# Optimization experiments

Measured on AMD Instinct MI355X. Metric: run time of the kernel, lower is better.

## Reference

```python
import jax, jax.numpy as jnp
import numpy as np

M = 131072  # KV length
DK = 256    # key dim
DV = 256    # value dim


def setup_inputs() -> dict:
    key = jax.random.key(0)
    k1, k2, k3 = jax.random.split(key, 3)
    q = jax.random.normal(k1, (DK,), dtype=jnp.float32)
    K = jax.random.normal(k2, (M, DK), dtype=jnp.float32)
    V = jax.random.normal(k3, (M, DV), dtype=jnp.float32)
    return {"q": q, "K": K, "V": V}


def reference(q, K, V):
    # logits[m] = sum_k K[m,k] * q[k]
    logits = jnp.einsum('mk,k->m', K, q)
    # stable softmax over the m axis
    weights = jax.nn.softmax(logits, axis=-1)
    # y[v] = sum_m weights[m] * V[m,v]
    return jnp.einsum('m,mv->v', weights, V)
```

## Files before the change

kernel.cpp:

```cpp
#include <hip/hip_runtime.h>
#include <math.h>

#define DKD 256
#define DVD 256

constexpr int NB_MAX = 1024;
constexpr int TPB    = 256;
constexpr int WAVES  = TPB / 64;
constexpr int RG     = 64;

__global__ __launch_bounds__(TPB) void attn_pass1(
    const float* __restrict__ q,
    const float* __restrict__ K,
    const float* __restrict__ V,
    float* __restrict__ m_arr,
    float* __restrict__ l_arr,
    float* __restrict__ acc_arr,
    int M, int rows_per_block)
{
    const int lane = threadIdx.x & 63;
    const int wave = threadIdx.x >> 6;
    const int b    = blockIdx.x;

    const float4* __restrict__ K4 = (const float4*)K;
    const float4* __restrict__ V4 = (const float4*)V;
    const float4  q4 = ((const float4*)q)[lane];

    const int row_begin = b * rows_per_block;
    const int row_end   = min(M, row_begin + rows_per_block);

    const int per_wave = (rows_per_block + WAVES - 1) / WAVES;
    const int wbeg = row_begin + wave * per_wave;
    const int wend = min(row_end, wbeg + per_wave);

    float  mx  = -INFINITY;
    float  l   = 0.0f;
    float4 acc = make_float4(0.f, 0.f, 0.f, 0.f);

    for (int r = wbeg; r < wend; r += 4) {
        const int r0 = r;
        const int r1 = min(r + 1, wend - 1);
        const int r2 = min(r + 2, wend - 1);
        const int r3 = min(r + 3, wend - 1);
        const bool v1 = (r + 1 < wend), v2 = (r + 2 < wend), v3 = (r + 3 < wend);

        float4 k0 = K4[(size_t)r0 * 64 + lane];
        float4 k1 = K4[(size_t)r1 * 64 + lane];
        float4 k2 = K4[(size_t)r2 * 64 + lane];
        float4 k3 = K4[(size_t)r3 * 64 + lane];
        float4 w0v = V4[(size_t)r0 * 64 + lane];
        float4 w1v = V4[(size_t)r1 * 64 + lane];
        float4 w2v = V4[(size_t)r2 * 64 + lane];
        float4 w3v = V4[(size_t)r3 * 64 + lane];

        float s0 = k0.x*q4.x + k0.y*q4.y + k0.z*q4.z + k0.w*q4.w;
        float s1 = k1.x*q4.x + k1.y*q4.y + k1.z*q4.z + k1.w*q4.w;
        float s2 = k2.x*q4.x + k2.y*q4.y + k2.z*q4.z + k2.w*q4.w;
        float s3 = k3.x*q4.x + k3.y*q4.y + k3.z*q4.z + k3.w*q4.w;

        #pragma unroll
        for (int off = 32; off > 0; off >>= 1) {
            s0 += __shfl_xor(s0, off);
            s1 += __shfl_xor(s1, off);
            s2 += __shfl_xor(s2, off);
            s3 += __shfl_xor(s3, off);
        }

        if (!v1) s1 = -INFINITY;
        if (!v2) s2 = -INFINITY;
        if (!v3) s3 = -INFINITY;

        const float nm = fmaxf(mx, fmaxf(fmaxf(s0, s1), fmaxf(s2, s3)));
        const float corr = __expf(mx - nm);
        const float e0 = __expf(s0 - nm);
        const float e1 = __expf(s1 - nm);
        const float e2 = __expf(s2 - nm);
        const float e3 = __expf(s3 - nm);

        l = l * corr + (e0 + e1 + e2 + e3);
        acc.x = acc.x * corr + e0*w0v.x + e1*w1v.x + e2*w2v.x + e3*w3v.x;
        acc.y = acc.y * corr + e0*w0v.y + e1*w1v.y + e2*w2v.y + e3*w3v.y;
        acc.z = acc.z * corr + e0*w0v.z + e1*w1v.z + e2*w2v.z + e3*w3v.z;
        acc.w = acc.w * corr + e0*w0v.w + e1*w1v.w + e2*w2v.w + e3*w3v.w;
        mx = nm;
    }

    __shared__ float4 s_acc[WAVES][64];
    __shared__ float  s_mx[WAVES];
    __shared__ float  s_l[WAVES];

    s_acc[wave][lane] = acc;
    if (lane == 0) { s_mx[wave] = mx; s_l[wave] = l; }
    __syncthreads();

    const int t = threadIdx.x;
    float bm = -INFINITY;
    #pragma unroll
    for (int w = 0; w < WAVES; ++w) bm = fmaxf(bm, s_mx[w]);
    if (bm == -INFINITY) bm = 0.0f;

    float yv = 0.0f, bl = 0.0f;
    const float* s_acc_f = (const float*)&s_acc[0][0];
    #pragma unroll
    for (int w = 0; w < WAVES; ++w) {
        const float sc = __expf(s_mx[w] - bm);
        yv += sc * s_acc_f[w * DVD + t];
        bl += sc * s_l[w];
    }

    acc_arr[(size_t)b * DVD + t] = yv;
    if (t == 0) { m_arr[b] = bm; l_arr[b] = bl; }
}

__global__ __launch_bounds__(256) void attn_pass2(
    const float* __restrict__ m_arr,
    const float* __restrict__ l_arr,
    const float* __restrict__ acc_arr,
    float* __restrict__ out,
    int nb, int chunk)
{
    __shared__ float red[256];
    __shared__ float sscale[64];
    const int t = threadIdx.x;

    float lm = -INFINITY;
    for (int b = t; b < nb; b += 256) lm = fmaxf(lm, m_arr[b]);
    red[t] = lm; __syncthreads();
    for (int s = 128; s > 0; s >>= 1) {
        if (t < s) red[t] = fmaxf(red[t], red[t + s]);
        __syncthreads();
    }
    const float Mg = red[0];
    __syncthreads();

    float ll = 0.0f;
    for (int b = t; b < nb; b += 256) ll += l_arr[b] * __expf(m_arr[b] - Mg);
    red[t] = ll; __syncthreads();
    for (int s = 128; s > 0; s >>= 1) {
        if (t < s) red[t] += red[t + s];
        __syncthreads();
    }
    const float invL = 1.0f / red[0];
    __syncthreads();

    const int b0 = blockIdx.x * chunk;
    const int b1 = min(nb, b0 + chunk);
    if (t < b1 - b0) sscale[t] = __expf(m_arr[b0 + t] - Mg);
    __syncthreads();

    float part = 0.0f;
    for (int b = b0; b < b1; ++b)
        part += sscale[b - b0] * acc_arr[(size_t)b * DVD + t];

    atomicAdd(&out[t], part * invL);
}

extern "C" void kernel_launch(void* const* d_in, const int* in_sizes, int n_in,
                              void* d_out, int out_size, void* d_ws, size_t ws_size,
                              hipStream_t stream) {
    const float* q = (const float*)d_in[0];
    const float* K = (const float*)d_in[1];
    const float* V = (const float*)d_in[2];
    float* out = (float*)d_out;

    const int M = in_sizes[1] / DKD;

    int nb = NB_MAX;
    while (nb > 1 && (size_t)nb * (2 + DVD) * sizeof(float) > ws_size) nb >>= 1;
    float* ws     = (float*)d_ws;
    float* m_arr  = ws;
    float* l_arr  = ws + nb;
    float* acc_arr= ws + 2 * nb;

    const int rpb = (M + nb - 1) / nb;

    hipMemsetAsync(d_out, 0, DVD * sizeof(float), stream);
    attn_pass1<<<nb, TPB, 0, stream>>>(q, K, V, m_arr, l_arr, acc_arr, M, rpb);
    const int chunk = (nb + RG - 1) / RG;
    attn_pass2<<<RG, 256, 0, stream>>>(m_arr, l_arr, acc_arr, out, nb, chunk);
}
```

Before: 287.1 us.

## Double block count, split remainder loop, and restructure final reduction per column

```diff
diff --git a/kernel.cpp b/kernel.cpp
--- a/kernel.cpp
+++ b/kernel.cpp
@@ -4,12 +4,11 @@
 #define DKD 256
 #define DVD 256
 
-constexpr int NB_MAX = 1024;
+constexpr int NB_MAX = 2048;
 constexpr int TPB    = 256;
 constexpr int WAVES  = TPB / 64;
-constexpr int RG     = 64;
 
-__global__ __launch_bounds__(TPB) void attn_pass1(
+__global__ __launch_bounds__(TPB, 8) void attn_pass1(
     const float* __restrict__ q,
     const float* __restrict__ K,
     const float* __restrict__ V,
@@ -37,21 +36,19 @@
     float  l   = 0.0f;
     float4 acc = make_float4(0.f, 0.f, 0.f, 0.f);
 
-    for (int r = wbeg; r < wend; r += 4) {
-        const int r0 = r;
-        const int r1 = min(r + 1, wend - 1);
-        const int r2 = min(r + 2, wend - 1);
-        const int r3 = min(r + 3, wend - 1);
-        const bool v1 = (r + 1 < wend), v2 = (r + 2 < wend), v3 = (r + 3 < wend);
+    const int n_rows = wend - wbeg;
+    const int full_end = wbeg + (n_rows & ~3);
 
-        float4 k0 = K4[(size_t)r0 * 64 + lane];
-        float4 k1 = K4[(size_t)r1 * 64 + lane];
-        float4 k2 = K4[(size_t)r2 * 64 + lane];
-        float4 k3 = K4[(size_t)r3 * 64 + lane];
-        float4 w0v = V4[(size_t)r0 * 64 + lane];
-        float4 w1v = V4[(size_t)r1 * 64 + lane];
-        float4 w2v = V4[(size_t)r2 * 64 + lane];
-        float4 w3v = V4[(size_t)r3 * 64 + lane];
+    for (int r = wbeg; r < full_end; r += 4) {
+        const size_t base = (size_t)r * 64 + lane;
+        float4 k0 = K4[base];
+        float4 k1 = K4[base + 64];
+        float4 k2 = K4[base + 128];
+        float4 k3 = K4[base + 192];
+        float4 v0 = V4[base];
+        float4 v1 = V4[base + 64];
+        float4 v2 = V4[base + 128];
+        float4 v3 = V4[base + 192];
 
         float s0 = k0.x*q4.x + k0.y*q4.y + k0.z*q4.z + k0.w*q4.w;
         float s1 = k1.x*q4.x + k1.y*q4.y + k1.z*q4.z + k1.w*q4.w;
@@ -66,10 +63,6 @@
             s3 += __shfl_xor(s3, off);
         }
 
-        if (!v1) s1 = -INFINITY;
-        if (!v2) s2 = -INFINITY;
-        if (!v3) s3 = -INFINITY;
-
         const float nm = fmaxf(mx, fmaxf(fmaxf(s0, s1), fmaxf(s2, s3)));
         const float corr = __expf(mx - nm);
         const float e0 = __expf(s0 - nm);
@@ -78,10 +71,27 @@
         const float e3 = __expf(s3 - nm);
 
         l = l * corr + (e0 + e1 + e2 + e3);
-        acc.x = acc.x * corr + e0*w0v.x + e1*w1v.x + e2*w2v.x + e3*w3v.x;
-        acc.y = acc.y * corr + e0*w0v.y + e1*w1v.y + e2*w2v.y + e3*w3v.y;
-        acc.z = acc.z * corr + e0*w0v.z + e1*w1v.z + e2*w2v.z + e3*w3v.z;
-        acc.w = acc.w * corr + e0*w0v.w + e1*w1v.w + e2*w2v.w + e3*w3v.w;
+        acc.x = acc.x * corr + e0*v0.x + e1*v1.x + e2*v2.x + e3*v3.x;
+        acc.y = acc.y * corr + e0*v0.y + e1*v1.y + e2*v2.y + e3*v3.y;
+        acc.z = acc.z * corr + e0*v0.z + e1*v1.z + e2*v2.z + e3*v3.z;
+        acc.w = acc.w * corr + e0*v0.w + e1*v1.w + e2*v2.w + e3*v3.w;
+        mx = nm;
+    }
+
+    for (int r = full_end; r < wend; ++r) {
+        float4 k0 = K4[(size_t)r * 64 + lane];
+        float4 v0 = V4[(size_t)r * 64 + lane];
+        float s0 = k0.x*q4.x + k0.y*q4.y + k0.z*q4.z + k0.w*q4.w;
+        #pragma unroll
+        for (int off = 32; off > 0; off >>= 1) s0 += __shfl_xor(s0, off);
+        const float nm = fmaxf(mx, s0);
+        const float corr = __expf(mx - nm);
+        const float e0 = __expf(s0 - nm);
+        l = l * corr + e0;
+        acc.x = acc.x * corr + e0*v0.x;
+        acc.y = acc.y * corr + e0*v0.y;
+        acc.z = acc.z * corr + e0*v0.z;
+        acc.w = acc.w * corr + e0*v0.w;
         mx = nm;
     }
 
@@ -117,10 +127,10 @@
     const float* __restrict__ l_arr,
     const float* __restrict__ acc_arr,
     float* __restrict__ out,
-    int nb, int chunk)
+    int nb)
 {
     __shared__ float red[256];
-    __shared__ float sscale[64];
+    __shared__ float sscale[NB_MAX];
     const int t = threadIdx.x;
 
     float lm = -INFINITY;
@@ -134,7 +144,11 @@
     __syncthreads();
 
     float ll = 0.0f;
-    for (int b = t; b < nb; b += 256) ll += l_arr[b] * __expf(m_arr[b] - Mg);
+    for (int b = t; b < nb; b += 256) {
+        const float sc = __expf(m_arr[b] - Mg);
+        sscale[b] = sc;
+        ll += sc * l_arr[b];
+    }
     red[t] = ll; __syncthreads();
     for (int s = 128; s > 0; s >>= 1) {
         if (t < s) red[t] += red[t + s];
@@ -143,16 +157,17 @@
     const float invL = 1.0f / red[0];
     __syncthreads();
 
-    const int b0 = blockIdx.x * chunk;
-    const int b1 = min(nb, b0 + chunk);
-    if (t < b1 - b0) sscale[t] = __expf(m_arr[b0 + t] - Mg);
-    __syncthreads();
+    const int j = blockIdx.x;
+    float part = 0.0f;
+    for (int b = t; b < nb; b += 256)
+        part += sscale[b] * acc_arr[(size_t)b * DVD + j];
 
-    float part = 0.0f;
-    for (int b = b0; b < b1; ++b)
-        part += sscale[b - b0] * acc_arr[(size_t)b * DVD + t];
-
-    atomicAdd(&out[t], part * invL);
+    red[t] = part; __syncthreads();
+    for (int s = 128; s > 0; s >>= 1) {
+        if (t < s) red[t] += red[t + s];
+        __syncthreads();
+    }
+    if (t == 0) out[j] = red[0] * invL;
 }
 
 extern "C" void kernel_launch(void* const* d_in, const int* in_sizes, int n_in,
@@ -167,15 +182,13 @@
 
     int nb = NB_MAX;
     while (nb > 1 && (size_t)nb * (2 + DVD) * sizeof(float) > ws_size) nb >>= 1;
-    float* ws     = (float*)d_ws;
-    float* m_arr  = ws;
-    float* l_arr  = ws + nb;
-    float* acc_arr= ws + 2 * nb;
+    float* ws      = (float*)d_ws;
+    float* m_arr   = ws;
+    float* l_arr   = ws + nb;
+    float* acc_arr = ws + 2 * nb;
 
     const int rpb = (M + nb - 1) / nb;
 
-    hipMemsetAsync(d_out, 0, DVD * sizeof(float), stream);
     attn_pass1<<<nb, TPB, 0, stream>>>(q, K, V, m_arr, l_arr, acc_arr, M, rpb);
-    const int chunk = (nb + RG - 1) / RG;
-    attn_pass2<<<RG, 256, 0, stream>>>(m_arr, l_arr, acc_arr, out, nb, chunk);
+    attn_pass2<<<DVD, 256, 0, stream>>>(m_arr, l_arr, acc_arr, out, nb);
 }
```

Result: no change. 286.7 us (-0.1%).
